# Optimization experiments

Measured on AMD Instinct MI355X. Metric: run time of the kernel, lower is better.

Reference implementation:

```python
import jax, jax.numpy as jnp
import numpy as np

BN_EPS = 1e-5
B, N1, N2, C = 4, 16384, 4096, 128
MLP = [256, 256]
IN_CH = 3 * C


def setup_inputs() -> dict:
    key = jax.random.key(0)
    ks = jax.random.split(key, 32)
    inp = {
        "xyz1": jax.random.normal(ks[0], (B, N1, 3), dtype=jnp.float32),
        "xyz2": jax.random.normal(ks[1], (B, N2, 3), dtype=jnp.float32),
        "points2": jax.random.normal(ks[2], (B, C, N2), dtype=jnp.float32),
        "points1": jax.random.normal(ks[3], (B, C, N1), dtype=jnp.float32),
        "points_b1": jax.random.normal(ks[4], (B, C, N1), dtype=jnp.float32),
    }
    ch = IN_CH
    k = 5
    for i, oc in enumerate(MLP):
        inp[f"w{i}"] = jax.random.normal(ks[k], (oc, ch), dtype=jnp.float32) / np.float32(np.sqrt(ch)); k += 1
        inp[f"b{i}"] = jnp.zeros((oc,), dtype=jnp.float32)
        inp[f"g{i}"] = jax.random.uniform(ks[k], (oc,), minval=0.5, maxval=1.5, dtype=jnp.float32); k += 1
        inp[f"beta{i}"] = 0.1 * jax.random.normal(ks[k], (oc,), dtype=jnp.float32); k += 1
        inp[f"m{i}"] = 0.1 * jax.random.normal(ks[k], (oc,), dtype=jnp.float32); k += 1
        inp[f"v{i}"] = jax.random.uniform(ks[k], (oc,), minval=0.5, maxval=1.5, dtype=jnp.float32); k += 1
        ch = oc
    return inp


def _conv_bn_relu(x, w, b, g, beta, m, v):
    # 1x1 conv over channel dim: x (B, Cin, N) -> (B, Cout, N), BN in eval mode, ReLU
    y = jnp.einsum("oc,bcn->bon", w, x) + b[None, :, None]
    y = (y - m[None, :, None]) * jax.lax.rsqrt(v[None, :, None] + BN_EPS) * g[None, :, None] + beta[None, :, None]
    return jax.nn.relu(y)


def reference(xyz1, xyz2, points2, points1, points_b1,
              w0, b0, g0, beta0, m0, v0,
              w1, b1, g1, beta1, m1, v1):
    # squared pairwise distances (B, N1, N2) via GEMM form
    d = (jnp.sum(xyz1 * xyz1, axis=-1)[:, :, None]
         + jnp.sum(xyz2 * xyz2, axis=-1)[:, None, :]
         - 2.0 * jnp.einsum("bnd,bmd->bnm", xyz1, xyz2))
    neg_d3, idx3 = jax.lax.top_k(-d, 3)              # 3 smallest distances
    d3 = -neg_d3                                      # (B, N1, 3)
    w = 1.0 / d3
    w = w / jnp.sum(w, axis=-1, keepdims=True)        # (B, N1, 3)
    p2t = jnp.transpose(points2, (0, 2, 1))           # (B, N2, C)
    gathered = jax.vmap(lambda p, i: p[i])(p2t, idx3) # (B, N1, 3, C)
    fused = jnp.einsum("bnk,bnkc->bcn", w, gathered)  # (B, C, N1)
    x = jnp.concatenate([points1, fused, points_b1], axis=1)  # (B, 3C, N1)
    x = _conv_bn_relu(x, w0, b0, g0, beta0, m0, v0)
    x = _conv_bn_relu(x, w1, b1, g1, beta1, m1, v1)
    return jnp.max(x, axis=1)                         # (B, N1)
```

## Files before the change

kernel.cpp:

```cpp
#include <hip/hip_runtime.h>

#define N1 16384
#define N2 4096
#define CC 128
#define KIN 384
#define HID 256

typedef unsigned short u16;
typedef unsigned int u32;

typedef _Float16 v8h __attribute__((ext_vector_type(8)));
typedef float v4f __attribute__((ext_vector_type(4)));


__device__ __forceinline__ u16 f2h(float f) {
    _Float16 h = (_Float16)f;
    return __builtin_bit_cast(u16, h);
}

__global__ __launch_bounds__(256) void prep_kernel(
    const float* __restrict__ w0, const float* __restrict__ w1,
    const float* __restrict__ b0, const float* __restrict__ g0, const float* __restrict__ be0,
    const float* __restrict__ m0, const float* __restrict__ v0,
    const float* __restrict__ b1, const float* __restrict__ g1, const float* __restrict__ be1,
    const float* __restrict__ m1, const float* __restrict__ v1,
    const float* __restrict__ xyz2,
    u16* __restrict__ W0h, u16* __restrict__ W1h,
    float* __restrict__ sst, float4* __restrict__ xyz2q)
{
    int id = blockIdx.x * 256 + threadIdx.x;
    if (id < 98304) {
        W0h[id] = f2h(w0[id]);
    } else if (id < 163840) {
        int t = id - 98304;
        W1h[t] = f2h(w1[t]);
    } else if (id < 164352) {
        int t = id - 163840;
        int o = t & 255;
        if (t < 256) {
            float s = g0[o] * rsqrtf(v0[o] + 1e-5f);
            sst[o]       = s;
            sst[256 + o] = (b0[o] - m0[o]) * s + be0[o];
        } else {
            float s = g1[o] * rsqrtf(v1[o] + 1e-5f);
            sst[512 + o] = s;
            sst[768 + o] = (b1[o] - m1[o]) * s + be1[o];
        }
    } else if (id < 180736) {
        int t = id - 164352;
        float x = xyz2[(size_t)t * 3 + 0];
        float y = xyz2[(size_t)t * 3 + 1];
        float z = xyz2[(size_t)t * 3 + 2];
        xyz2q[t] = make_float4(x, y, z, fmaf(x, x, fmaf(y, y, z * z)));
    }
}

__global__ __launch_bounds__(256) void transpose_kernel(
    const float* __restrict__ points2, float* __restrict__ p2t)
{
    __shared__ float tile[64][129];
    int n20 = blockIdx.x * 64;
    int b   = blockIdx.y;
    int tid = threadIdx.x;

    int jr = tid & 63, cr = tid >> 6;
#pragma unroll 8
    for (int it = 0; it < 32; ++it) {
        int ch = it * 4 + cr;
        tile[jr][ch] = points2[((size_t)b * CC + ch) * N2 + n20 + jr];
    }
    __syncthreads();

    int cw = tid & 127, jw0 = tid >> 7;
#pragma unroll 8
    for (int it = 0; it < 32; ++it) {
        int j = it * 2 + jw0;
        p2t[((size_t)b * N2 + n20 + j) * CC + cw] = tile[j][cw];
    }
}

#define BINS(t, cand, D0, D1, D2, I0, I1, I2) do {                    \
    bool c0 = (t) < (D0);                                             \
    bool c1 = (t) < (D1);                                             \
    bool c2 = (t) < (D2);                                             \
    I2 = c1 ? (I1) : (c2 ? (cand) : (I2));                \
    I1 = c0 ? (I0) : (c1 ? (cand) : (I1));                \
    I0 = c0 ? (cand) : (I0);                                          \
    D2 = __builtin_amdgcn_fmed3f((D1), (t), (D2));        \
    D1 = __builtin_amdgcn_fmed3f((D0), (t), (D1));        \
    D0 = fminf((t), (D0));                                            \
} while (0)

#define INS3LEX(t, j, D0, D1, D2, I0, I1, I2) do {                    \
    bool lt2 = (t) < (D2) || ((t) == (D2) && (j) < (I2));             \
    bool lt1 = (t) < (D1) || ((t) == (D1) && (j) < (I1));             \
    bool lt0 = (t) < (D0) || ((t) == (D0) && (j) < (I0));             \
    if (lt2) {                                                        \
        if (lt1) {                                                    \
            D2 = (D1); I2 = (I1);                                     \
            if (lt0) { D1 = (D0); I1 = (I0); D0 = (t); I0 = (j); }    \
            else     { D1 = (t); I1 = (j); }                          \
        } else { D2 = (t); I2 = (j); }                                \
    }                                                                 \
} while (0)

#define MERGE_STEP(st, D0, D1, D2, I0, I1, I2) do {                   \
    float e0 = __shfl_xor((D0), (st), 64);                            \
    float e1 = __shfl_xor((D1), (st), 64);                            \
    float e2 = __shfl_xor((D2), (st), 64);                            \
    int   j0 = __shfl_xor((I0), (st), 64);                            \
    int   j1 = __shfl_xor((I1), (st), 64);                            \
    int   j2 = __shfl_xor((I2), (st), 64);                            \
    INS3LEX(e0, j0, D0, D1, D2, I0, I1, I2);                          \
    INS3LEX(e1, j1, D0, D1, D2, I0, I1, I2);                          \
    INS3LEX(e2, j2, D0, D1, D2, I0, I1, I2);                          \
} while (0)

#define KNN_OUT(Q, D0, D1, D2, I0, I1, I2, PP) do {                   \
    float r0 = 1.f / ((D0) + (PP));                                   \
    float r1 = 1.f / ((D1) + (PP));                                   \
    float r2 = 1.f / ((D2) + (PP));                                   \
    float inv = 1.f / (r0 + r1 + r2);                                 \
    size_t o3 = ((size_t)b * N1 + p0 + (Q)) * 3;                      \
    idx3[o3]     = (I0);                                              \
    idx3[o3 + 1] = (I1);                                              \
    idx3[o3 + 2] = (I2);                                              \
    w3[o3]     = r0 * inv;                                            \
    w3[o3 + 1] = r1 * inv;                                            \
    w3[o3 + 2] = r2 * inv;                                            \
} while (0)

__global__ __launch_bounds__(256)
__attribute__((amdgpu_waves_per_eu(8, 8)))
void knn_kernel(
    const float* __restrict__ xyz1, const float4* __restrict__ xyz2q,
    int* __restrict__ idx3, float* __restrict__ w3)
{
    __shared__ float4 slds[1024];

    int tid = threadIdx.x;
    int b   = blockIdx.y;
    int n0  = blockIdx.x * 32;

    int s  = tid & 15;
    int g  = tid >> 4;
    int p0 = n0 + g * 2;

    size_t pb = ((size_t)b * N1 + p0) * 3;
    float x0 = xyz1[pb + 0], y0 = xyz1[pb + 1], z0 = xyz1[pb + 2];
    float x1 = xyz1[pb + 3], y1 = xyz1[pb + 4], z1 = xyz1[pb + 5];
    float ax0 = -2.f * x0, ay0 = -2.f * y0, az0 = -2.f * z0;
    float ax1 = -2.f * x1, ay1 = -2.f * y1, az1 = -2.f * z1;
    float pp0 = fmaf(x0, x0, fmaf(y0, y0, z0 * z0));
    float pp1 = fmaf(x1, x1, fmaf(y1, y1, z1 * z1));

    float da0 = 1e30f, da1 = 1e30f, da2 = 1e30f;
    float db0 = 1e30f, db1 = 1e30f, db2 = 1e30f;
    int   ia0 = 0, ia1 = 0, ia2 = 0;
    int   ib0 = 0, ib1 = 0, ib2 = 0;

#pragma unroll
    for (int stage = 0; stage < 4; ++stage) {
        int base = stage * 1024;
#pragma unroll
        for (int i = 0; i < 4; ++i)
            slds[tid + i * 256] = xyz2q[(size_t)b * N2 + base + tid + i * 256];
        __syncthreads();

#pragma unroll 4
        for (int k = 0; k < 64; ++k) {
            int c = s + (k << 4);
            float4 v = slds[c];
            int cand = base + c;
            float t0 = fmaf(ax0, v.x, fmaf(ay0, v.y, fmaf(az0, v.z, v.w)));
            float t1 = fmaf(ax1, v.x, fmaf(ay1, v.y, fmaf(az1, v.z, v.w)));
            BINS(t0, cand, da0, da1, da2, ia0, ia1, ia2);
            BINS(t1, cand, db0, db1, db2, ib0, ib1, ib2);
        }
        __syncthreads();
    }

#pragma unroll
    for (int st = 1; st <= 8; st <<= 1) {
        MERGE_STEP(st, da0, da1, da2, ia0, ia1, ia2);
        MERGE_STEP(st, db0, db1, db2, ib0, ib1, ib2);
    }

    if (s == 0) {
        KNN_OUT(0, da0, da1, da2, ia0, ia1, ia2, pp0);
        KNN_OUT(1, db0, db1, db2, ib0, ib1, ib2, pp1);
    }
}

__global__ __launch_bounds__(256)
__attribute__((amdgpu_waves_per_eu(5, 5)))
void mlp_kernel(
    const float* __restrict__ points1, const float* __restrict__ pointsb1,
    const float4* __restrict__ p2t4,
    const int* __restrict__ idx3, const float* __restrict__ w3,
    const uint4* __restrict__ W0v, const uint4* __restrict__ W1v,
    const float* __restrict__ sst, float* __restrict__ out)
{
    __shared__ __align__(16) u16 sx[32 * KIN];
    __shared__ float sred[4][32];
    __shared__ int   s_idx[96];
    __shared__ float s_w[96];

    int tid = threadIdx.x;
    int b   = blockIdx.y;
    int n0  = blockIdx.x * 32;

    if (tid < 96) {
        size_t gi = ((size_t)b * N1 + n0) * 3 + tid;
        s_idx[tid] = idx3[gi];
        s_w[tid]   = w3[gi];
    }

    int pL = tid & 31;
    int t4 = (tid >> 5) * 4;
#pragma unroll
    for (int k = 0; k < 4; ++k) {
        int r4 = t4 + 32 * k;
        size_t base = ((size_t)b * CC + r4) * N1 + n0 + pL;
        float a0 = points1[base];
        float a1 = points1[base + (size_t)N1];
        float a2 = points1[base + (size_t)2 * N1];
        float a3 = points1[base + (size_t)3 * N1];
        u32 lo = f2h(a0) | ((u32)f2h(a1) << 16);
        u32 hi = f2h(a2) | ((u32)f2h(a3) << 16);
        int chunk = (r4 >> 3) ^ (pL & 7);
        *(uint2*)&sx[pL * KIN + chunk * 8 + (r4 & 7)] = make_uint2(lo, hi);
    }
#pragma unroll
    for (int k = 0; k < 4; ++k) {
        int r4 = t4 + 32 * k;
        int k4 = 256 + r4;
        size_t base = ((size_t)b * CC + r4) * N1 + n0 + pL;
        float a0 = pointsb1[base];
        float a1 = pointsb1[base + (size_t)N1];
        float a2 = pointsb1[base + (size_t)2 * N1];
        float a3 = pointsb1[base + (size_t)3 * N1];
        u32 lo = f2h(a0) | ((u32)f2h(a1) << 16);
        u32 hi = f2h(a2) | ((u32)f2h(a3) << 16);
        int chunk = (k4 >> 3) ^ (pL & 7);
        *(uint2*)&sx[pL * KIN + chunk * 8 + (k4 & 7)] = make_uint2(lo, hi);
    }
    __syncthreads();

    int c4  = tid & 31;
    int pg  = tid >> 5;
    int k4g = 128 + c4 * 4;
#pragma unroll
    for (int k = 0; k < 4; ++k) {
        int p = pg + 8 * k;
        float w0w = s_w[p * 3 + 0], w1w = s_w[p * 3 + 1], w2w = s_w[p * 3 + 2];
        float4 f0 = p2t4[((size_t)b * N2 + s_idx[p * 3 + 0]) * 32 + c4];
        float4 f1 = p2t4[((size_t)b * N2 + s_idx[p * 3 + 1]) * 32 + c4];
        float4 f2 = p2t4[((size_t)b * N2 + s_idx[p * 3 + 2]) * 32 + c4];
        float e0 = fmaf(w0w, f0.x, fmaf(w1w, f1.x, w2w * f2.x));
        float e1 = fmaf(w0w, f0.y, fmaf(w1w, f1.y, w2w * f2.y));
        float e2 = fmaf(w0w, f0.z, fmaf(w1w, f1.z, w2w * f2.z));
        float e3 = fmaf(w0w, f0.w, fmaf(w1w, f1.w, w2w * f2.w));
        u32 lo = f2h(e0) | ((u32)f2h(e1) << 16);
        u32 hi = f2h(e2) | ((u32)f2h(e3) << 16);
        int chunk = (k4g >> 3) ^ (p & 7);
        *(uint2*)&sx[p * KIN + chunk * 8 + (k4g & 7)] = make_uint2(lo, hi);
    }
    __syncthreads();

    int lane = tid & 63, w = tid >> 6;
    int ml = lane & 15, ql = lane >> 4;
    int px7 = ml & 7;

    v4f acc1[4][2];
#pragma unroll
    for (int ot = 0; ot < 4; ++ot)
        for (int pt = 0; pt < 2; ++pt)
            acc1[ot][pt] = (v4f){0.f, 0.f, 0.f, 0.f};

#pragma unroll
    for (int s = 0; s < 12; ++s) {
        int kc = s * 4 + ql;
        int pc = (kc ^ px7) * 8;
        v8h bf0 = __builtin_bit_cast(v8h, *(const uint4*)&sx[ml * KIN + pc]);
        v8h bf1 = __builtin_bit_cast(v8h, *(const uint4*)&sx[(16 + ml) * KIN + pc]);
#pragma unroll
        for (int ot = 0; ot < 4; ++ot) {
            int o = w * 64 + ot * 16 + ml;
            v8h af = __builtin_bit_cast(v8h, W0v[o * 48 + kc]);
            acc1[ot][0] = __builtin_amdgcn_mfma_f32_16x16x32_f16(af, bf0, acc1[ot][0], 0, 0, 0);
            acc1[ot][1] = __builtin_amdgcn_mfma_f32_16x16x32_f16(af, bf1, acc1[ot][1], 0, 0, 0);
        }
    }
    __syncthreads();

    const float* s0v = sst;
    const float* t0v = sst + 256;
#pragma unroll
    for (int ot = 0; ot < 4; ++ot) {
        int o0 = w * 64 + ot * 16 + ql * 4;
        float sc0 = s0v[o0], sc1 = s0v[o0 + 1], sc2 = s0v[o0 + 2], sc3 = s0v[o0 + 3];
        float sh0 = t0v[o0], sh1 = t0v[o0 + 1], sh2 = t0v[o0 + 2], sh3 = t0v[o0 + 3];
        int chunk = ((o0 >> 3) ^ px7);
#pragma unroll
        for (int pt = 0; pt < 2; ++pt) {
            int p = pt * 16 + ml;
            float z0 = fmaxf(fmaf(acc1[ot][pt][0], sc0, sh0), 0.f);
            float z1 = fmaxf(fmaf(acc1[ot][pt][1], sc1, sh1), 0.f);
            float z2 = fmaxf(fmaf(acc1[ot][pt][2], sc2, sh2), 0.f);
            float z3 = fmaxf(fmaf(acc1[ot][pt][3], sc3, sh3), 0.f);
            u32 lo = f2h(z0) | ((u32)f2h(z1) << 16);
            u32 hi = f2h(z2) | ((u32)f2h(z3) << 16);
            *(uint2*)&sx[p * HID + chunk * 8 + (o0 & 7)] = make_uint2(lo, hi);
        }
    }
    __syncthreads();

    v4f acc2[4][2];
#pragma unroll
    for (int ot = 0; ot < 4; ++ot)
        for (int pt = 0; pt < 2; ++pt)
            acc2[ot][pt] = (v4f){0.f, 0.f, 0.f, 0.f};

#pragma unroll
    for (int s = 0; s < 8; ++s) {
        int kc = s * 4 + ql;
        int pc = (kc ^ px7) * 8;
        v8h bf0 = __builtin_bit_cast(v8h, *(const uint4*)&sx[ml * HID + pc]);
        v8h bf1 = __builtin_bit_cast(v8h, *(const uint4*)&sx[(16 + ml) * HID + pc]);
#pragma unroll
        for (int ot = 0; ot < 4; ++ot) {
            int o = w * 64 + ot * 16 + ml;
            v8h af = __builtin_bit_cast(v8h, W1v[o * 32 + kc]);
            acc2[ot][0] = __builtin_amdgcn_mfma_f32_16x16x32_f16(af, bf0, acc2[ot][0], 0, 0, 0);
            acc2[ot][1] = __builtin_amdgcn_mfma_f32_16x16x32_f16(af, bf1, acc2[ot][1], 0, 0, 0);
        }
    }

    const float* s1v = sst + 512;
    const float* t1v = sst + 768;
    float mx0 = 0.f, mx1 = 0.f;
#pragma unroll
    for (int ot = 0; ot < 4; ++ot) {
        int o0 = w * 64 + ot * 16 + ql * 4;
#pragma unroll
        for (int r = 0; r < 4; ++r) {
            float sc = s1v[o0 + r], sh = t1v[o0 + r];
            mx0 = fmaxf(mx0, fmaf(acc2[ot][0][r], sc, sh));
            mx1 = fmaxf(mx1, fmaf(acc2[ot][1][r], sc, sh));
        }
    }
    mx0 = fmaxf(mx0, __shfl_xor(mx0, 16, 64));
    mx0 = fmaxf(mx0, __shfl_xor(mx0, 32, 64));
    mx1 = fmaxf(mx1, __shfl_xor(mx1, 16, 64));
    mx1 = fmaxf(mx1, __shfl_xor(mx1, 32, 64));
    if (lane < 16) {
        sred[w][ml]      = mx0;
        sred[w][16 + ml] = mx1;
    }
    __syncthreads();
    if (tid < 32)
        out[(size_t)b * N1 + n0 + tid] =
            fmaxf(fmaxf(sred[0][tid], sred[1][tid]),
                  fmaxf(sred[2][tid], sred[3][tid]));
}

extern "C" void kernel_launch(void* const* d_in, const int* in_sizes, int n_in,
                              void* d_out, int out_size, void* d_ws, size_t ws_size,
                              hipStream_t stream)
{
    const float* xyz1     = (const float*)d_in[0];
    const float* xyz2     = (const float*)d_in[1];
    const float* points2  = (const float*)d_in[2];
    const float* points1  = (const float*)d_in[3];
    const float* pointsb1 = (const float*)d_in[4];
    const float* w0   = (const float*)d_in[5];
    const float* b0   = (const float*)d_in[6];
    const float* g0   = (const float*)d_in[7];
    const float* be0  = (const float*)d_in[8];
    const float* m0   = (const float*)d_in[9];
    const float* v0   = (const float*)d_in[10];
    const float* w1   = (const float*)d_in[11];
    const float* b1   = (const float*)d_in[12];
    const float* g1   = (const float*)d_in[13];
    const float* be1  = (const float*)d_in[14];
    const float* m1   = (const float*)d_in[15];
    const float* v1   = (const float*)d_in[16];
    float* out = (float*)d_out;

    char* ws = (char*)d_ws;
    u16*    W0h   = (u16*)(ws + 0);
    u16*    W1h   = (u16*)(ws + 196608);
    float*  sst   = (float*)(ws + 327680);
    float4* xyz2q = (float4*)(ws + 331776);
    int*    idx3  = (int*)(ws + 593920);
    float*  w3    = (float*)(ws + 1380352);
    float*  p2t   = (float*)(ws + 2166784);

    prep_kernel<<<706, 256, 0, stream>>>(w0, w1, b0, g0, be0, m0, v0,
                                         b1, g1, be1, m1, v1, xyz2,
                                         W0h, W1h, sst, xyz2q);
    transpose_kernel<<<dim3(64, 4), 256, 0, stream>>>(points2, p2t);
    knn_kernel<<<dim3(512, 4), 256, 0, stream>>>(xyz1, xyz2q, idx3, w3);
    mlp_kernel<<<dim3(512, 4), 256, 0, stream>>>(points1, pointsb1,
                                                 (const float4*)p2t, idx3, w3,
                                                 (const uint4*)W0h, (const uint4*)W1h,
                                                 sst, out);
}
```

Before: 321.5 us.

## Replace brute-force KNN with x-sorted candidates and pruned bidirectional sweep

Adds a per-batch bitonic sort of xyz2 by x coordinate, then has each query binary-search its x position and scan outward in both directions with two threads, stopping once the x-gap squared exceeds the current third-best distance. This aims to remove most of the O(N1*N2) distance evaluations of the brute-force kernel. The cost is a new serial single-block-per-batch sort launch, data-dependent divergent loops, and a tie-handling path. Pruning effectiveness depends on the point distribution.

```diff
diff --git a/kernel.cpp b/kernel.cpp
--- a/kernel.cpp
+++ b/kernel.cpp
@@ -24,9 +24,8 @@
     const float* __restrict__ m0, const float* __restrict__ v0,
     const float* __restrict__ b1, const float* __restrict__ g1, const float* __restrict__ be1,
     const float* __restrict__ m1, const float* __restrict__ v1,
-    const float* __restrict__ xyz2,
     u16* __restrict__ W0h, u16* __restrict__ W1h,
-    float* __restrict__ sst, float4* __restrict__ xyz2q)
+    float* __restrict__ sst)
 {
     int id = blockIdx.x * 256 + threadIdx.x;
     if (id < 98304) {
@@ -46,12 +45,49 @@
             sst[512 + o] = s;
             sst[768 + o] = (b1[o] - m1[o]) * s + be1[o];
         }
-    } else if (id < 180736) {
-        int t = id - 164352;
-        float x = xyz2[(size_t)t * 3 + 0];
-        float y = xyz2[(size_t)t * 3 + 1];
-        float z = xyz2[(size_t)t * 3 + 2];
-        xyz2q[t] = make_float4(x, y, z, fmaf(x, x, fmaf(y, y, z * z)));
+    }
+}
+
+__global__ __launch_bounds__(1024) void sort_kernel(
+    const float* __restrict__ xyz2, uint4* __restrict__ S)
+{
+    __shared__ float sx[4096];
+    __shared__ u16   si[4096];
+    int b   = blockIdx.x;
+    int tid = threadIdx.x;
+
+    for (int i = tid; i < 4096; i += 1024) {
+        sx[i] = xyz2[((size_t)b * 4096 + i) * 3];
+        si[i] = (u16)i;
+    }
+
+    for (int k = 2; k <= 4096; k <<= 1) {
+        for (int j = k >> 1; j > 0; j >>= 1) {
+            __syncthreads();
+            for (int t = tid; t < 4096; t += 1024) {
+                int ixj = t ^ j;
+                if (ixj > t) {
+                    float a = sx[t], c = sx[ixj];
+                    bool up = ((t & k) == 0);
+                    if (up ? (a > c) : (a < c)) {
+                        sx[t] = c; sx[ixj] = a;
+                        u16 tmp = si[t]; si[t] = si[ixj]; si[ixj] = tmp;
+                    }
+                }
+            }
+        }
+    }
+    __syncthreads();
+
+    for (int i = tid; i < 4096; i += 1024) {
+        int sidx = si[i];
+        size_t base = ((size_t)b * 4096 + sidx) * 3;
+        uint4 o;
+        o.x = __builtin_bit_cast(u32, sx[i]);
+        o.y = __builtin_bit_cast(u32, xyz2[base + 1]);
+        o.z = __builtin_bit_cast(u32, xyz2[base + 2]);
+        o.w = (u32)sidx;
+        S[(size_t)b * 4096 + i] = o;
     }
 }
 
@@ -116,79 +152,85 @@
     INS3LEX(e2, j2, D0, D1, D2, I0, I1, I2);                          \
 } while (0)
 
-#define KNN_OUT(Q, D0, D1, D2, I0, I1, I2, PP) do {                   \
-    float r0 = 1.f / ((D0) + (PP));                                   \
-    float r1 = 1.f / ((D1) + (PP));                                   \
-    float r2 = 1.f / ((D2) + (PP));                                   \
-    float inv = 1.f / (r0 + r1 + r2);                                 \
-    size_t o3 = ((size_t)b * N1 + p0 + (Q)) * 3;                      \
-    idx3[o3]     = (I0);                                              \
-    idx3[o3 + 1] = (I1);                                              \
-    idx3[o3 + 2] = (I2);                                              \
-    w3[o3]     = r0 * inv;                                            \
-    w3[o3 + 1] = r1 * inv;                                            \
-    w3[o3 + 2] = r2 * inv;                                            \
+#define PROC(c, vld) do {                                             \
+    float cc_ = fmaf((c).x, (c).x, fmaf((c).y, (c).y, (c).z * (c).z));\
+    float t_  = fmaf(ax, (c).x, fmaf(ay, (c).y, fmaf(az, (c).z, cc_)));\
+    if (!(vld)) t_ = 3e38f;                                           \
+    int  ci_ = __builtin_bit_cast(int, (c).w);                        \
+    bool eq_ = (t_ == da0) || (t_ == da1) || (t_ == da2);             \
+    if (__any(eq_)) { INS3LEX(t_, ci_, da0, da1, da2, ia0, ia1, ia2); }\
+    else            { BINS(t_, ci_, da0, da1, da2, ia0, ia1, ia2); }  \
 } while (0)
 
 __global__ __launch_bounds__(256)
-__attribute__((amdgpu_waves_per_eu(8, 8)))
 void knn_kernel(
-    const float* __restrict__ xyz1, const float4* __restrict__ xyz2q,
+    const float* __restrict__ xyz1, const uint4* __restrict__ S,
     int* __restrict__ idx3, float* __restrict__ w3)
 {
-    __shared__ float4 slds[1024];
-
-    int tid = threadIdx.x;
-    int b   = blockIdx.y;
-    int n0  = blockIdx.x * 32;
-
-    int s  = tid & 15;
-    int g  = tid >> 4;
-    int p0 = n0 + g * 2;
-
-    size_t pb = ((size_t)b * N1 + p0) * 3;
-    float x0 = xyz1[pb + 0], y0 = xyz1[pb + 1], z0 = xyz1[pb + 2];
-    float x1 = xyz1[pb + 3], y1 = xyz1[pb + 4], z1 = xyz1[pb + 5];
-    float ax0 = -2.f * x0, ay0 = -2.f * y0, az0 = -2.f * z0;
-    float ax1 = -2.f * x1, ay1 = -2.f * y1, az1 = -2.f * z1;
-    float pp0 = fmaf(x0, x0, fmaf(y0, y0, z0 * z0));
-    float pp1 = fmaf(x1, x1, fmaf(y1, y1, z1 * z1));
+    __shared__ __align__(16) float4 sc[4096];
+
+    int tid  = threadIdx.x;
+    int b    = blockIdx.y;
+    int qloc = tid >> 1;
+    int side = tid & 1;
+    int n    = blockIdx.x * 128 + qloc;
+
+    const uint4* Sb = S + (size_t)b * 4096;
+#pragma unroll
+    for (int i = 0; i < 16; ++i)
+        *(uint4*)&sc[tid + i * 256] = Sb[tid + i * 256];
+
+    size_t pb = ((size_t)b * N1 + n) * 3;
+    float qx = xyz1[pb], qy = xyz1[pb + 1], qz = xyz1[pb + 2];
+    float ax = -2.f * qx, ay = -2.f * qy, az = -2.f * qz;
+    float pp = fmaf(qx, qx, fmaf(qy, qy, qz * qz));
+    __syncthreads();
+
+    int lo = 0, hi = 4096;
+    while (lo < hi) {
+        int mid = (lo + hi) >> 1;
+        if (sc[mid].x < qx) lo = mid + 1; else hi = mid;
+    }
 
     float da0 = 1e30f, da1 = 1e30f, da2 = 1e30f;
-    float db0 = 1e30f, db1 = 1e30f, db2 = 1e30f;
     int   ia0 = 0, ia1 = 0, ia2 = 0;
-    int   ib0 = 0, ib1 = 0, ib2 = 0;
-
-#pragma unroll
-    for (int stage = 0; stage < 4; ++stage) {
-        int base = stage * 1024;
-#pragma unroll
-        for (int i = 0; i < 4; ++i)
-            slds[tid + i * 256] = xyz2q[(size_t)b * N2 + base + tid + i * 256];
-        __syncthreads();
-
-#pragma unroll 4
-        for (int k = 0; k < 64; ++k) {
-            int c = s + (k << 4);
-            float4 v = slds[c];
-            int cand = base + c;
-            float t0 = fmaf(ax0, v.x, fmaf(ay0, v.y, fmaf(az0, v.z, v.w)));
-            float t1 = fmaf(ax1, v.x, fmaf(ay1, v.y, fmaf(az1, v.z, v.w)));
-            BINS(t0, cand, da0, da1, da2, ia0, ia1, ia2);
-            BINS(t1, cand, db0, db1, db2, ib0, ib1, ib2);
-        }
-        __syncthreads();
-    }
-
-#pragma unroll
-    for (int st = 1; st <= 8; st <<= 1) {
-        MERGE_STEP(st, da0, da1, da2, ia0, ia1, ia2);
-        MERGE_STEP(st, db0, db1, db2, ib0, ib1, ib2);
-    }
-
-    if (s == 0) {
-        KNN_OUT(0, da0, da1, da2, ia0, ia1, ia2, pp0);
-        KNN_OUT(1, db0, db1, db2, ib0, ib1, ib2, pp1);
+
+    int  dstep = side ? -4 : 4;
+    int  ptr   = side ? lo - 4 : lo;
+    bool act   = side ? (ptr + 3 >= 0) : (ptr <= 4095);
+
+    while (__any(act)) {
+        if (act) {
+            int i0 = ptr, i1 = ptr + 1, i2 = ptr + 2, i3 = ptr + 3;
+            float4 c0 = sc[i0 & 4095];
+            float4 c1 = sc[i1 & 4095];
+            float4 c2 = sc[i2 & 4095];
+            float4 c3 = sc[i3 & 4095];
+            bool v0 = (u32)i0 < 4096u;
+            bool v1 = (u32)i1 < 4096u;
+            bool v2 = (u32)i2 < 4096u;
+            bool v3 = (u32)i3 < 4096u;
+            PROC(c0, v0); PROC(c1, v1); PROC(c2, v2); PROC(c3, v3);
+            float dxn = side ? (qx - c3.x) : (c0.x - qx);
+            act = !(fmaf(dxn, dxn, -pp) > da2 + 1e-3f);
+            ptr += dstep;
+            act = act && (side ? (ptr + 3 >= 0) : (ptr <= 4095));
+        }
+    }
+
+    MERGE_STEP(1, da0, da1, da2, ia0, ia1, ia2);
+    if (side == 0) {
+        float r0 = 1.f / (da0 + pp);
+        float r1 = 1.f / (da1 + pp);
+        float r2 = 1.f / (da2 + pp);
+        float inv = 1.f / (r0 + r1 + r2);
+        size_t o3 = ((size_t)b * N1 + n) * 3;
+        idx3[o3]     = ia0;
+        idx3[o3 + 1] = ia1;
+        idx3[o3 + 2] = ia2;
+        w3[o3]     = r0 * inv;
+        w3[o3 + 1] = r1 * inv;
+        w3[o3 + 2] = r2 * inv;
     }
 }
 
@@ -392,16 +434,17 @@
     u16*    W0h   = (u16*)(ws + 0);
     u16*    W1h   = (u16*)(ws + 196608);
     float*  sst   = (float*)(ws + 327680);
-    float4* xyz2q = (float4*)(ws + 331776);
+    uint4*  S     = (uint4*)(ws + 331776);
     int*    idx3  = (int*)(ws + 593920);
     float*  w3    = (float*)(ws + 1380352);
     float*  p2t   = (float*)(ws + 2166784);
 
-    prep_kernel<<<706, 256, 0, stream>>>(w0, w1, b0, g0, be0, m0, v0,
-                                         b1, g1, be1, m1, v1, xyz2,
-                                         W0h, W1h, sst, xyz2q);
+    prep_kernel<<<642, 256, 0, stream>>>(w0, w1, b0, g0, be0, m0, v0,
+                                         b1, g1, be1, m1, v1,
+                                         W0h, W1h, sst);
+    sort_kernel<<<4, 1024, 0, stream>>>(xyz2, S);
     transpose_kernel<<<dim3(64, 4), 256, 0, stream>>>(points2, p2t);
-    knn_kernel<<<dim3(512, 4), 256, 0, stream>>>(xyz1, xyz2q, idx3, w3);
+    knn_kernel<<<dim3(128, 4), 256, 0, stream>>>(xyz1, S, idx3, w3);
     mlp_kernel<<<dim3(512, 4), 256, 0, stream>>>(points1, pointsb1,
                                                  (const float4*)p2t, idx3, w3,
                                                  (const uint4*)W0h, (const uint4*)W1h,
```

Measured after the change: 743.2 us. 131% more time.
